# Kernel tuning notes

Measured on AMD Instinct MI355X. Metric: run time of the kernel, lower is better.

The kernel has to match this reference:

```python
import jax, jax.numpy as jnp
import numpy as np

V = 20000   # input_size (POI vocab)
U = 10000   # user_count
H = 128     # hidden_size
B = 64      # user_len (batch)
S = 200     # seq_len
LAM_T = 0.01
LAM_S = 100.0
DAY = 86400.0


def setup_inputs() -> dict:
    key = jax.random.key(0)
    ks = jax.random.split(key, 12)
    sc = 1.0 / np.sqrt(H)
    return {
        "poi_inputs": jax.random.randint(ks[0], (B, S), 0, V),
        "lengths": jnp.full((B,), S, dtype=jnp.int32),  # full sequences -> pack/pad is identity
        "timestamp_inputs": jnp.sort(jax.random.uniform(ks[1], (B, S), minval=0.0, maxval=DAY), axis=1),
        "location_inputs": jax.random.normal(ks[2], (B, S, 2)) * 0.1,
        "active_user": jax.random.randint(ks[3], (B,), 0, U),
        "emb_W": jax.random.normal(ks[4], (V, H)),      # nn.Embedding default N(0,1)
        "user_W": jax.random.normal(ks[5], (U, H)),
        "W_ih": jax.random.uniform(ks[6], (H, H), minval=-sc, maxval=sc),
        "W_hh": jax.random.uniform(ks[7], (H, H), minval=-sc, maxval=sc),
        "b_ih": jax.random.uniform(ks[8], (H,), minval=-sc, maxval=sc),
        "b_hh": jax.random.uniform(ks[9], (H,), minval=-sc, maxval=sc),
        "fc_W": jax.random.uniform(ks[10], (V, 2 * H), minval=-sc, maxval=sc),  # torch Linear [out,in]
        "fc_b": jax.random.uniform(ks[11], (V,), minval=-sc, maxval=sc),
    }


def _safe_norm(d):
    # norm over last axis with zero (not nan) gradient at d == 0
    d2 = jnp.sum(d * d, axis=-1)
    pos = d2 > 0
    return jnp.where(pos, jnp.sqrt(jnp.where(pos, d2, 1.0)), 0.0)


def reference(poi_inputs, lengths, timestamp_inputs, location_inputs, active_user,
              emb_W, user_W, W_ih, W_hh, b_ih, b_hh, fc_W, fc_b):
    t, s = timestamp_inputs, location_inputs
    x_emb = emb_W[poi_inputs]                       # [B,S,H]

    # vanilla tanh RNN (torch nn.RNN, batch_first) via scan over time
    def step(h, xt):
        h = jnp.tanh(xt @ W_ih.T + b_ih + h @ W_hh.T + b_hh)
        return h, h
    h0 = jnp.zeros((x_emb.shape[0], W_hh.shape[0]), x_emb.dtype)
    _, out = jax.lax.scan(step, h0, jnp.swapaxes(x_emb, 0, 1))
    out = jnp.swapaxes(out, 0, 1)                   # [B,S,H]

    # vectorized spatio-temporal decay attention (original O(S^2) python loop)
    dt = jnp.maximum(t[:, :, None] - t[:, None, :], 0.0)          # [B,S,S] clamp_min(0)
    ds = _safe_norm(s[:, :, None, :] - s[:, None, :, :])          # [B,S,S]
    a_j = ((jnp.cos(dt * (2.0 * jnp.pi / DAY)) + 1.0) * 0.5) * jnp.exp(-dt * LAM_T)
    b_j = jnp.exp(-ds * LAM_S)
    causal = jnp.tril(jnp.ones((t.shape[1], t.shape[1]), bool))   # j <= i
    w = jnp.where(causal, a_j * b_j + 1e-10, 0.0)                 # [B,S,S]
    sum_w = jnp.maximum(jnp.sum(w, axis=-1), 1e-10)               # [B,S]
    out_w = jnp.einsum('bij,bjh->bih', w, out) / sum_w[..., None] # [B,S,H]

    p_u = jnp.broadcast_to(user_W[active_user][:, None, :], out_w.shape)
    out_pu = jnp.concatenate([out_w, p_u], axis=-1)               # [B,S,2H]
    y = jax.nn.softmax(out_pu @ fc_W.T + fc_b, axis=-1)           # [B,S,V]
    return y, out_pu
```

## Files before the change

kernel.cpp:

```cpp
#include <hip/hip_runtime.h>
#include <hip/hip_bf16.h>
#include <stdint.h>

#define B_   64
#define S_   200
#define H_   128
#define V_   20000
#define M_   12800
#define NPAD 20224
#define NBN  158
#define NBM  100
#define NWG2 15800

#define WS_A      0u
#define WS_FCW    3276800u
#define WS_U      8454144u
#define WS_RSUM   13631488u
#define WS_WTIH   13682688u

#define XP_OFF    0
#define HOUT_OFF  2000000
#define PART_OFF  4000000
#define OUTPU_OFF 256000000ll

typedef __attribute__((ext_vector_type(8))) __bf16 bf16x8;
typedef __attribute__((ext_vector_type(4))) float  f32x4;

__device__ __forceinline__ void gll16(const void* g, void* l) {
  __builtin_amdgcn_global_load_lds(
      (const __attribute__((address_space(1))) void*)g,
      (__attribute__((address_space(3))) void*)l, 16, 0, 0);
}

__global__ __launch_bounds__(256)
void prep_w1(const float* __restrict__ fcw, __hip_bfloat16* __restrict__ w1) {
  int t = threadIdx.x;
  int row = blockIdx.x * 2 + (t >> 7);
  int col = t & 127;
  float v = (row < V_) ? fcw[(long)row * 256 + col] : 0.f;
  w1[(long)row * 128 + col] = __float2bfloat16(v);
}

__global__ __launch_bounds__(128)
void prep_wt(const float* __restrict__ w_ih, float* __restrict__ wt) {
  int bid = blockIdx.x, t = threadIdx.x;
  wt[bid * 128 + t] = w_ih[t * 128 + bid];
}

__global__ __launch_bounds__(256)
void user_k(const int* __restrict__ auser, const float* __restrict__ userW,
            const float* __restrict__ fcW, const float* __restrict__ fcb,
            float* __restrict__ U) {
  __shared__ float uw[8][128];
  int t = threadIdx.x;
  int c = blockIdx.x * 256 + t;
  int b0 = blockIdx.y * 8;
  for (int i = t; i < 8 * 128; i += 256) {
    int bb = i >> 7, kk = i & 127;
    uw[bb][kk] = userW[(long)auser[b0 + bb] * 128 + kk];
  }
  __syncthreads();
  float acc[8];
#pragma unroll
  for (int bb = 0; bb < 8; ++bb) acc[bb] = 0.f;
  if (c < V_) {
    const float* w2 = fcW + (long)c * 256 + 128;
    for (int kq = 0; kq < 32; ++kq) {
      float4 wv = *(const float4*)(w2 + 4 * kq);
#pragma unroll
      for (int bb = 0; bb < 8; ++bb) {
        float4 uv = *(const float4*)&uw[bb][4 * kq];
        acc[bb] = fmaf(wv.x, uv.x, acc[bb]);
        acc[bb] = fmaf(wv.y, uv.y, acc[bb]);
        acc[bb] = fmaf(wv.z, uv.z, acc[bb]);
        acc[bb] = fmaf(wv.w, uv.w, acc[bb]);
      }
    }
    float base = fcb[c];
#pragma unroll
    for (int bb = 0; bb < 8; ++bb)
      U[(long)(b0 + bb) * NPAD + c] = base + acc[bb];
  } else {
#pragma unroll
    for (int bb = 0; bb < 8; ++bb)
      U[(long)(b0 + bb) * NPAD + c] = -1e30f;
  }
}

__global__ __launch_bounds__(128)
void xproj_k(const int* __restrict__ poi, const float* __restrict__ emb,
             const float* __restrict__ wt_ih, const float* __restrict__ b_ih,
             const float* __restrict__ b_hh, float* __restrict__ xp) {
  __shared__ float xs[16][128];
  int j = threadIdx.x;
  int m0 = blockIdx.x * 16;
#pragma unroll
  for (int i = 0; i < 16; ++i)
    xs[i][j] = emb[(long)poi[m0 + i] * 128 + j];
  __syncthreads();
  float bias = b_ih[j] + b_hh[j];
  float acc[16];
#pragma unroll
  for (int i = 0; i < 16; ++i) acc[i] = bias;
  for (int kq = 0; kq < 32; ++kq) {
    float w0 = wt_ih[(4 * kq + 0) * 128 + j];
    float w1 = wt_ih[(4 * kq + 1) * 128 + j];
    float w2 = wt_ih[(4 * kq + 2) * 128 + j];
    float w3 = wt_ih[(4 * kq + 3) * 128 + j];
#pragma unroll
    for (int i = 0; i < 16; ++i) {
      float4 xv = *(const float4*)&xs[i][4 * kq];
      acc[i] = fmaf(xv.x, w0, acc[i]);
      acc[i] = fmaf(xv.y, w1, acc[i]);
      acc[i] = fmaf(xv.z, w2, acc[i]);
      acc[i] = fmaf(xv.w, w3, acc[i]);
    }
  }
#pragma unroll
  for (int i = 0; i < 16; ++i)
    xp[(long)(m0 + i) * 128 + j] = acc[i];
}

__global__ __launch_bounds__(128)
void rnn_k(const float* __restrict__ xp, const float* __restrict__ w_hh,
           float* __restrict__ hout) {
  int b = blockIdx.x, j = threadIdx.x;
  float w[128];
#pragma unroll
  for (int k = 0; k < 128; ++k) w[k] = w_hh[j * 128 + k];
  __shared__ float hs[2][128];
  hs[0][j] = 0.f;
  __syncthreads();
  int cur = 0;
  for (int t = 0; t < S_; ++t) {
    float x0 = xp[((long)b * S_ + t) * 128 + j];
    const float4* hp4 = (const float4*)hs[cur];
    float a0 = 0.f, a1 = 0.f, a2 = 0.f, a3 = 0.f;
#pragma unroll
    for (int k = 0; k < 8; ++k) {
      float4 v0 = hp4[k], v1 = hp4[k + 8], v2 = hp4[k + 16], v3 = hp4[k + 24];
      a0 = fmaf(v0.x, w[4 * k + 0], a0); a0 = fmaf(v0.y, w[4 * k + 1], a0);
      a0 = fmaf(v0.z, w[4 * k + 2], a0); a0 = fmaf(v0.w, w[4 * k + 3], a0);
      a1 = fmaf(v1.x, w[32 + 4 * k + 0], a1); a1 = fmaf(v1.y, w[32 + 4 * k + 1], a1);
      a1 = fmaf(v1.z, w[32 + 4 * k + 2], a1); a1 = fmaf(v1.w, w[32 + 4 * k + 3], a1);
      a2 = fmaf(v2.x, w[64 + 4 * k + 0], a2); a2 = fmaf(v2.y, w[64 + 4 * k + 1], a2);
      a2 = fmaf(v2.z, w[64 + 4 * k + 2], a2); a2 = fmaf(v2.w, w[64 + 4 * k + 3], a2);
      a3 = fmaf(v3.x, w[96 + 4 * k + 0], a3); a3 = fmaf(v3.y, w[96 + 4 * k + 1], a3);
      a3 = fmaf(v3.z, w[96 + 4 * k + 2], a3); a3 = fmaf(v3.w, w[96 + 4 * k + 3], a3);
    }
    float hn = tanhf(x0 + ((a0 + a1) + (a2 + a3)));
    hs[cur ^ 1][j] = hn;
    hout[((long)b * S_ + t) * 128 + j] = hn;
    cur ^= 1;
    __syncthreads();
  }
}

__global__ __launch_bounds__(128)
void attn_k(const float* __restrict__ ts, const float* __restrict__ loc,
            const float* __restrict__ hout, const int* __restrict__ auser,
            const float* __restrict__ userW, float* __restrict__ outpu,
            __hip_bfloat16* __restrict__ Abf) {
  int i = blockIdx.x, b = blockIdx.y, h = threadIdx.x;
  __shared__ float wl[128];
  const float OMEGA = 7.27220521664304e-05f;
  float ti = ts[b * S_ + i];
  float lx = loc[(b * S_ + i) * 2 + 0];
  float ly = loc[(b * S_ + i) * 2 + 1];
  float acc = 0.f, sw = 0.f;
  for (int jc = 0; jc <= i; jc += 128) {
    int j = jc + h;
    float wj = 0.f;
    if (j <= i) {
      float dt = fmaxf(ti - ts[b * S_ + j], 0.f);
      float a = (cosf(dt * OMEGA) + 1.f) * 0.5f * expf(-dt * 0.01f);
      float dx = lx - loc[(b * S_ + j) * 2 + 0];
      float dy = ly - loc[(b * S_ + j) * 2 + 1];
      float dn = sqrtf(dx * dx + dy * dy);
      wj = a * expf(-dn * 100.f) + 1e-10f;
    }
    __syncthreads();
    wl[h] = wj;
    __syncthreads();
    int lim = min(128, i - jc + 1);
    const float* hb = hout + ((long)b * S_ + jc) * 128 + h;
    int jj = 0;
    for (; jj + 4 <= lim; jj += 4) {
      float4 wv4 = *(const float4*)&wl[jj];
      float h0 = hb[(long)(jj + 0) * 128];
      float h1 = hb[(long)(jj + 1) * 128];
      float h2 = hb[(long)(jj + 2) * 128];
      float h3 = hb[(long)(jj + 3) * 128];
      acc = fmaf(wv4.x, h0, acc); sw += wv4.x;
      acc = fmaf(wv4.y, h1, acc); sw += wv4.y;
      acc = fmaf(wv4.z, h2, acc); sw += wv4.z;
      acc = fmaf(wv4.w, h3, acc); sw += wv4.w;
    }
    for (; jj < lim; ++jj) {
      float wv = wl[jj];
      acc = fmaf(wv, hb[(long)jj * 128], acc);
      sw += wv;
    }
  }
  float ow = acc / fmaxf(sw, 1e-10f);
  long m = (long)b * S_ + i;
  float pu = userW[(long)auser[b] * 128 + h];
  outpu[m * 256 + h]       = ow;
  outpu[m * 256 + 128 + h] = pu;
  Abf[m * 128 + h]         = __float2bfloat16(ow);
}

template <int PASS>
__global__ __launch_bounds__(512, 4)
void gemm_fc(const __hip_bfloat16* __restrict__ A,
             const __hip_bfloat16* __restrict__ Bw,
             const float* __restrict__ Ut,
             const float* __restrict__ rowsum,
             float* __restrict__ part,
             float* __restrict__ y) {
  __shared__ __align__(16) char smem[65536];
  __shared__ float rsum4[4][128];
  char* AsB = smem;
  char* BsB = smem + 32768;
  float* lbuf = (float*)smem;

  const int tid  = threadIdx.x;
  const int lane = tid & 63;
  const int wid  = tid >> 6;
  const int wr = wid >> 2, wc = wid & 3;
  const int g = lane >> 4, lr = lane & 15;

  const int orig = blockIdx.x;
  const int nid = (orig & 7) * (NWG2 / 8) + (orig >> 3);
  const int bm = nid / NBN, bn = nid % NBN;
  const long brow = (long)bm * 128, bcol = (long)bn * 128;

  const char* Ab = (const char*)A + brow * 256;
  const char* Bb = (const char*)Bw + bcol * 256;

#pragma unroll
  for (int i = 0; i < 4; ++i) {
    int ci = i * 512 + tid;
    int row = ci >> 4;
    int w = (ci & 15) ^ (row & 7);
    long src = (long)row * 256 + (long)w * 16;
    gll16(Ab + src, AsB + (long)ci * 16);
    gll16(Bb + src, BsB + (long)ci * 16);
  }
  __syncthreads();

  f32x4 acc[4][2];
#pragma unroll
  for (int mi = 0; mi < 4; ++mi)
#pragma unroll
    for (int ni = 0; ni < 2; ++ni) acc[mi][ni] = (f32x4)(0.f);

#pragma unroll
  for (int kk = 0; kk < 4; ++kk) {
    bf16x8 af[4], bfr[2];
#pragma unroll
    for (int mi = 0; mi < 4; ++mi) {
      int row = wr * 64 + mi * 16 + lr;
      int w = ((kk << 2) | g) ^ (row & 7);
      af[mi] = *(const bf16x8*)(AsB + row * 256 + w * 16);
    }
#pragma unroll
    for (int ni = 0; ni < 2; ++ni) {
      int row = wc * 32 + ni * 16 + lr;
      int w = ((kk << 2) | g) ^ (row & 7);
      bfr[ni] = *(const bf16x8*)(BsB + row * 256 + w * 16);
    }
#pragma unroll
    for (int mi = 0; mi < 4; ++mi)
#pragma unroll
      for (int ni = 0; ni < 2; ++ni)
        acc[mi][ni] = __builtin_amdgcn_mfma_f32_16x16x32_bf16(af[mi], bfr[ni], acc[mi][ni], 0, 0, 0);
  }

  if (PASS == 0) {
#pragma unroll
    for (int mi = 0; mi < 4; ++mi) {
#pragma unroll
      for (int r = 0; r < 4; ++r) {
        long row = brow + wr * 64 + mi * 16 + g * 4 + r;
        const float* urow = Ut + (long)(row / S_) * NPAD + bcol;
        float s = 0.f;
#pragma unroll
        for (int ni = 0; ni < 2; ++ni) {
          float u = urow[wc * 32 + ni * 16 + lr];
          s += __expf(acc[mi][ni][r] + u);
        }
#pragma unroll
        for (int off = 1; off < 16; off <<= 1) s += __shfl_xor(s, off);
        if (lr == 0) rsum4[wc][wr * 64 + mi * 16 + g * 4 + r] = s;
      }
    }
    __syncthreads();
    if (tid < 128)
      part[(long)bn * M_ + brow + tid] =
          rsum4[0][tid] + rsum4[1][tid] + rsum4[2][tid] + rsum4[3][tid];
  } else {
    if (bcol >= V_) return;
    const bool full = (bcol + 128 <= V_);
    __syncthreads();
#pragma unroll
    for (int mi = 0; mi < 4; ++mi) {
#pragma unroll
      for (int r = 0; r < 4; ++r) {
        int lrow = wr * 64 + mi * 16 + g * 4 + r;
        long row = brow + lrow;
        const float* urow = Ut + (long)(row / S_) * NPAD + bcol;
        float inv = 1.0f / rowsum[row];
        int key = ((lrow >> 2) & 3) << 2;
#pragma unroll
        for (int ni = 0; ni < 2; ++ni) {
          int lcol = wc * 32 + ni * 16 + lr;
          lbuf[lrow * 128 + (lcol ^ key)] = __expf(acc[mi][ni][r] + urow[lcol]) * inv;
        }
      }
    }
    __syncthreads();
    if (full) {
#pragma unroll
      for (int it = 0; it < 8; ++it) {
        int idx = it * 512 + tid;
        int lrow = idx >> 5, c4 = idx & 31;
        int key = ((lrow >> 2) & 3) << 2;
        f32x4 v = *(const f32x4*)(lbuf + lrow * 128 + ((c4 * 4) ^ key));
        __builtin_nontemporal_store(v,
            (f32x4*)(y + (brow + lrow) * (long)V_ + bcol + c4 * 4));
      }
    } else {
#pragma unroll
      for (int it = 0; it < 8; ++it) {
        int idx = it * 512 + tid;
        int lrow = idx >> 5, c4 = idx & 31;
        int key = ((lrow >> 2) & 3) << 2;
        const float* src = lbuf + lrow * 128 + ((c4 * 4) ^ key);
        long row = brow + lrow;
#pragma unroll
        for (int e = 0; e < 4; ++e) {
          int col = (int)bcol + c4 * 4 + e;
          if (col < V_) y[row * (long)V_ + col] = src[e];
        }
      }
    }
  }
}

__global__ void reduce_rows(const float* __restrict__ part, float* __restrict__ rowsum) {
  int m = blockIdx.x * 256 + threadIdx.x;
  if (m < M_) {
    float s = 0.f;
    for (int bn = 0; bn < NBN; ++bn) s += part[(long)bn * M_ + m];
    rowsum[m] = fmaxf(s, 1e-30f);
  }
}

extern "C" void kernel_launch(void* const* d_in, const int* in_sizes, int n_in,
                              void* d_out, int out_size, void* d_ws, size_t ws_size,
                              hipStream_t stream) {
  const int*   poi   = (const int*)d_in[0];
  const float* ts    = (const float*)d_in[2];
  const float* loc   = (const float*)d_in[3];
  const int*   auser = (const int*)d_in[4];
  const float* embW  = (const float*)d_in[5];
  const float* userW = (const float*)d_in[6];
  const float* w_ih  = (const float*)d_in[7];
  const float* w_hh  = (const float*)d_in[8];
  const float* b_ih  = (const float*)d_in[9];
  const float* b_hh  = (const float*)d_in[10];
  const float* fcW   = (const float*)d_in[11];
  const float* fcb   = (const float*)d_in[12];

  float* out = (float*)d_out;
  char*  ws  = (char*)d_ws;
  __hip_bfloat16* Abf    = (__hip_bfloat16*)(ws + WS_A);
  __hip_bfloat16* w1b    = (__hip_bfloat16*)(ws + WS_FCW);
  float*          Ut     = (float*)(ws + WS_U);
  float*          rowsum = (float*)(ws + WS_RSUM);
  float*          wt_ih  = (float*)(ws + WS_WTIH);

  float* xp    = out + XP_OFF;
  float* hout  = out + HOUT_OFF;
  float* part  = out + PART_OFF;
  float* outpu = out + OUTPU_OFF;

  prep_w1<<<dim3(NPAD / 2), dim3(256), 0, stream>>>(fcW, w1b);
  prep_wt<<<dim3(128), dim3(128), 0, stream>>>(w_ih, wt_ih);
  user_k<<<dim3(NPAD / 256, 8), dim3(256), 0, stream>>>(auser, userW, fcW, fcb, Ut);
  xproj_k<<<dim3(M_ / 16), dim3(128), 0, stream>>>(poi, embW, wt_ih, b_ih, b_hh, xp);
  rnn_k<<<dim3(B_), dim3(128), 0, stream>>>(xp, w_hh, hout);
  attn_k<<<dim3(S_, B_), dim3(128), 0, stream>>>(ts, loc, hout, auser, userW, outpu, Abf);
  gemm_fc<0><<<dim3(NWG2), dim3(512), 0, stream>>>(Abf, w1b, Ut, nullptr, part, nullptr);
  reduce_rows<<<dim3(50), dim3(256), 0, stream>>>(part, rowsum);
  gemm_fc<1><<<dim3(NWG2), dim3(512), 0, stream>>>(Abf, w1b, Ut, rowsum, nullptr, out);
}
```

Before: 762.6 us.

## Tile attention over 8 query rows with shared-memory hidden tile; remap GEMM block order

```diff
diff --git a/kernel.cpp b/kernel.cpp
--- a/kernel.cpp
+++ b/kernel.cpp
@@ -11,6 +11,7 @@
 #define NBN  158
 #define NBM  100
 #define NWG2 15800
+#define TI   8
 
 #define WS_A      0u
 #define WS_FCW    3276800u
@@ -161,53 +162,69 @@
             const float* __restrict__ hout, const int* __restrict__ auser,
             const float* __restrict__ userW, float* __restrict__ outpu,
             __hip_bfloat16* __restrict__ Abf) {
-  int i = blockIdx.x, b = blockIdx.y, h = threadIdx.x;
-  __shared__ float wl[128];
+  int it = blockIdx.x, b = blockIdx.y, h = threadIdx.x;
+  int i0 = it * TI;
+  __shared__ float htile[128 * 128];
+  __shared__ float wls[TI][128];
   const float OMEGA = 7.27220521664304e-05f;
-  float ti = ts[b * S_ + i];
-  float lx = loc[(b * S_ + i) * 2 + 0];
-  float ly = loc[(b * S_ + i) * 2 + 1];
-  float acc = 0.f, sw = 0.f;
-  for (int jc = 0; jc <= i; jc += 128) {
+  float ti[TI], lx[TI], ly[TI], acc[TI], sw[TI];
+#pragma unroll
+  for (int ii = 0; ii < TI; ++ii) {
+    ti[ii] = ts[b * S_ + i0 + ii];
+    lx[ii] = loc[(b * S_ + i0 + ii) * 2 + 0];
+    ly[ii] = loc[(b * S_ + i0 + ii) * 2 + 1];
+    acc[ii] = 0.f; sw[ii] = 0.f;
+  }
+  for (int jc = 0; jc < i0 + TI; jc += 128) {
+    int nrows = min(128, i0 + TI - jc);
+    __syncthreads();
+    {
+      const float4* src = (const float4*)(hout + ((long)b * S_ + jc) * 128);
+      float4* dst = (float4*)htile;
+      int n4 = nrows * 32;
+      for (int idx = h; idx < n4; idx += 128) dst[idx] = src[idx];
+    }
     int j = jc + h;
-    float wj = 0.f;
-    if (j <= i) {
-      float dt = fmaxf(ti - ts[b * S_ + j], 0.f);
-      float a = (cosf(dt * OMEGA) + 1.f) * 0.5f * expf(-dt * 0.01f);
-      float dx = lx - loc[(b * S_ + j) * 2 + 0];
-      float dy = ly - loc[(b * S_ + j) * 2 + 1];
-      float dn = sqrtf(dx * dx + dy * dy);
-      wj = a * expf(-dn * 100.f) + 1e-10f;
-    }
-    __syncthreads();
-    wl[h] = wj;
-    __syncthreads();
-    int lim = min(128, i - jc + 1);
-    const float* hb = hout + ((long)b * S_ + jc) * 128 + h;
-    int jj = 0;
-    for (; jj + 4 <= lim; jj += 4) {
-      float4 wv4 = *(const float4*)&wl[jj];
-      float h0 = hb[(long)(jj + 0) * 128];
-      float h1 = hb[(long)(jj + 1) * 128];
-      float h2 = hb[(long)(jj + 2) * 128];
-      float h3 = hb[(long)(jj + 3) * 128];
-      acc = fmaf(wv4.x, h0, acc); sw += wv4.x;
-      acc = fmaf(wv4.y, h1, acc); sw += wv4.y;
-      acc = fmaf(wv4.z, h2, acc); sw += wv4.z;
-      acc = fmaf(wv4.w, h3, acc); sw += wv4.w;
-    }
-    for (; jj < lim; ++jj) {
-      float wv = wl[jj];
-      acc = fmaf(wv, hb[(long)jj * 128], acc);
-      sw += wv;
-    }
-  }
-  float ow = acc / fmaxf(sw, 1e-10f);
-  long m = (long)b * S_ + i;
+    float tj = ts[b * S_ + j < B_ * S_ ? b * S_ + j : 0];
+    float jx = 0.f, jy = 0.f;
+    if (j < S_) {
+      tj = ts[b * S_ + j];
+      jx = loc[(b * S_ + j) * 2 + 0];
+      jy = loc[(b * S_ + j) * 2 + 1];
+    }
+#pragma unroll
+    for (int ii = 0; ii < TI; ++ii) {
+      float wj = 0.f;
+      if (j <= i0 + ii) {
+        float dt = fmaxf(ti[ii] - tj, 0.f);
+        float a = (cosf(dt * OMEGA) + 1.f) * 0.5f * expf(-dt * 0.01f);
+        float dx = lx[ii] - jx;
+        float dy = ly[ii] - jy;
+        float dn = sqrtf(dx * dx + dy * dy);
+        wj = a * expf(-dn * 100.f) + 1e-10f;
+      }
+      wls[ii][h] = wj;
+    }
+    __syncthreads();
+#pragma unroll
+    for (int ii = 0; ii < TI; ++ii) {
+      int lim = min(nrows, i0 + ii - jc + 1);
+      for (int r = 0; r < lim; ++r) {
+        float wv = wls[ii][r];
+        acc[ii] = fmaf(wv, htile[r * 128 + h], acc[ii]);
+        sw[ii] += wv;
+      }
+    }
+  }
   float pu = userW[(long)auser[b] * 128 + h];
-  outpu[m * 256 + h]       = ow;
-  outpu[m * 256 + 128 + h] = pu;
-  Abf[m * 128 + h]         = __float2bfloat16(ow);
+#pragma unroll
+  for (int ii = 0; ii < TI; ++ii) {
+    long m = (long)b * S_ + i0 + ii;
+    float ow = acc[ii] / fmaxf(sw[ii], 1e-10f);
+    outpu[m * 256 + h]       = ow;
+    outpu[m * 256 + 128 + h] = pu;
+    Abf[m * 128 + h]         = __float2bfloat16(ow);
+  }
 }
 
 template <int PASS>
@@ -232,7 +249,7 @@
 
   const int orig = blockIdx.x;
   const int nid = (orig & 7) * (NWG2 / 8) + (orig >> 3);
-  const int bm = nid / NBN, bn = nid % NBN;
+  const int bn = nid / NBM, bm = nid % NBM;
   const long brow = (long)bm * 128, bcol = (long)bn * 128;
 
   const char* Ab = (const char*)A + brow * 256;
@@ -391,7 +408,7 @@
   user_k<<<dim3(NPAD / 256, 8), dim3(256), 0, stream>>>(auser, userW, fcW, fcb, Ut);
   xproj_k<<<dim3(M_ / 16), dim3(128), 0, stream>>>(poi, embW, wt_ih, b_ih, b_hh, xp);
   rnn_k<<<dim3(B_), dim3(128), 0, stream>>>(xp, w_hh, hout);
-  attn_k<<<dim3(S_, B_), dim3(128), 0, stream>>>(ts, loc, hout, auser, userW, outpu, Abf);
+  attn_k<<<dim3(S_ / TI, B_), dim3(128), 0, stream>>>(ts, loc, hout, auser, userW, outpu, Abf);
   gemm_fc<0><<<dim3(NWG2), dim3(512), 0, stream>>>(Abf, w1b, Ut, nullptr, part, nullptr);
   reduce_rows<<<dim3(50), dim3(256), 0, stream>>>(part, rowsum);
   gemm_fc<1><<<dim3(NWG2), dim3(512), 0, stream>>>(Abf, w1b, Ut, rowsum, nullptr, out);
```

Result: slower. 797.5 us (+4.6%).

## Fuse RNN, weight bf16 conversion and user projection into one heterogeneous launch

Applied to the files above, without the earlier changes.

```diff
diff --git a/kernel.cpp b/kernel.cpp
--- a/kernel.cpp
+++ b/kernel.cpp
@@ -32,59 +32,10 @@
       (__attribute__((address_space(3))) void*)l, 16, 0, 0);
 }
 
-__global__ __launch_bounds__(256)
-void prep_w1(const float* __restrict__ fcw, __hip_bfloat16* __restrict__ w1) {
-  int t = threadIdx.x;
-  int row = blockIdx.x * 2 + (t >> 7);
-  int col = t & 127;
-  float v = (row < V_) ? fcw[(long)row * 256 + col] : 0.f;
-  w1[(long)row * 128 + col] = __float2bfloat16(v);
-}
-
 __global__ __launch_bounds__(128)
 void prep_wt(const float* __restrict__ w_ih, float* __restrict__ wt) {
   int bid = blockIdx.x, t = threadIdx.x;
   wt[bid * 128 + t] = w_ih[t * 128 + bid];
-}
-
-__global__ __launch_bounds__(256)
-void user_k(const int* __restrict__ auser, const float* __restrict__ userW,
-            const float* __restrict__ fcW, const float* __restrict__ fcb,
-            float* __restrict__ U) {
-  __shared__ float uw[8][128];
-  int t = threadIdx.x;
-  int c = blockIdx.x * 256 + t;
-  int b0 = blockIdx.y * 8;
-  for (int i = t; i < 8 * 128; i += 256) {
-    int bb = i >> 7, kk = i & 127;
-    uw[bb][kk] = userW[(long)auser[b0 + bb] * 128 + kk];
-  }
-  __syncthreads();
-  float acc[8];
-#pragma unroll
-  for (int bb = 0; bb < 8; ++bb) acc[bb] = 0.f;
-  if (c < V_) {
-    const float* w2 = fcW + (long)c * 256 + 128;
-    for (int kq = 0; kq < 32; ++kq) {
-      float4 wv = *(const float4*)(w2 + 4 * kq);
-#pragma unroll
-      for (int bb = 0; bb < 8; ++bb) {
-        float4 uv = *(const float4*)&uw[bb][4 * kq];
-        acc[bb] = fmaf(wv.x, uv.x, acc[bb]);
-        acc[bb] = fmaf(wv.y, uv.y, acc[bb]);
-        acc[bb] = fmaf(wv.z, uv.z, acc[bb]);
-        acc[bb] = fmaf(wv.w, uv.w, acc[bb]);
-      }
-    }
-    float base = fcb[c];
-#pragma unroll
-    for (int bb = 0; bb < 8; ++bb)
-      U[(long)(b0 + bb) * NPAD + c] = base + acc[bb];
-  } else {
-#pragma unroll
-    for (int bb = 0; bb < 8; ++bb)
-      U[(long)(b0 + bb) * NPAD + c] = -1e30f;
-  }
 }
 
 __global__ __launch_bounds__(128)
@@ -121,38 +72,105 @@
     xp[(long)(m0 + i) * 128 + j] = acc[i];
 }
 
-__global__ __launch_bounds__(128)
-void rnn_k(const float* __restrict__ xp, const float* __restrict__ w_hh,
-           float* __restrict__ hout) {
-  int b = blockIdx.x, j = threadIdx.x;
-  float w[128];
-#pragma unroll
-  for (int k = 0; k < 128; ++k) w[k] = w_hh[j * 128 + k];
-  __shared__ float hs[2][128];
-  hs[0][j] = 0.f;
-  __syncthreads();
-  int cur = 0;
-  for (int t = 0; t < S_; ++t) {
-    float x0 = xp[((long)b * S_ + t) * 128 + j];
-    const float4* hp4 = (const float4*)hs[cur];
-    float a0 = 0.f, a1 = 0.f, a2 = 0.f, a3 = 0.f;
-#pragma unroll
-    for (int k = 0; k < 8; ++k) {
-      float4 v0 = hp4[k], v1 = hp4[k + 8], v2 = hp4[k + 16], v3 = hp4[k + 24];
-      a0 = fmaf(v0.x, w[4 * k + 0], a0); a0 = fmaf(v0.y, w[4 * k + 1], a0);
-      a0 = fmaf(v0.z, w[4 * k + 2], a0); a0 = fmaf(v0.w, w[4 * k + 3], a0);
-      a1 = fmaf(v1.x, w[32 + 4 * k + 0], a1); a1 = fmaf(v1.y, w[32 + 4 * k + 1], a1);
-      a1 = fmaf(v1.z, w[32 + 4 * k + 2], a1); a1 = fmaf(v1.w, w[32 + 4 * k + 3], a1);
-      a2 = fmaf(v2.x, w[64 + 4 * k + 0], a2); a2 = fmaf(v2.y, w[64 + 4 * k + 1], a2);
-      a2 = fmaf(v2.z, w[64 + 4 * k + 2], a2); a2 = fmaf(v2.w, w[64 + 4 * k + 3], a2);
-      a3 = fmaf(v3.x, w[96 + 4 * k + 0], a3); a3 = fmaf(v3.y, w[96 + 4 * k + 1], a3);
-      a3 = fmaf(v3.z, w[96 + 4 * k + 2], a3); a3 = fmaf(v3.w, w[96 + 4 * k + 3], a3);
-    }
-    float hn = tanhf(x0 + ((a0 + a1) + (a2 + a3)));
-    hs[cur ^ 1][j] = hn;
-    hout[((long)b * S_ + t) * 128 + j] = hn;
-    cur ^= 1;
-    __syncthreads();
+__global__ __launch_bounds__(256)
+void fused_pre(const float* __restrict__ xp, const float* __restrict__ w_hh,
+               float* __restrict__ hout,
+               const float* __restrict__ fcW, __hip_bfloat16* __restrict__ w1,
+               const int* __restrict__ auser, const float* __restrict__ userW,
+               const float* __restrict__ fcb, float* __restrict__ U) {
+  __shared__ float smem_u[8][128];
+  int blk = blockIdx.x;
+  int t = threadIdx.x;
+
+  if (blk < 64) {
+    int b = blk, j = t & 127;
+    float* hs = (float*)smem_u;
+    float w[128];
+#pragma unroll
+    for (int k = 0; k < 128; ++k) w[k] = w_hh[j * 128 + k];
+    hs[j] = 0.f;
+    __syncthreads();
+    int cur = 0;
+    for (int tt = 0; tt < S_; ++tt) {
+      float x0 = xp[((long)b * S_ + tt) * 128 + j];
+      const float4* hp4 = (const float4*)(hs + cur * 128);
+      float a0 = 0.f, a1 = 0.f, a2 = 0.f, a3 = 0.f;
+#pragma unroll
+      for (int k = 0; k < 8; ++k) {
+        float4 v0 = hp4[k], v1 = hp4[k + 8], v2 = hp4[k + 16], v3 = hp4[k + 24];
+        a0 = fmaf(v0.x, w[4 * k + 0], a0); a0 = fmaf(v0.y, w[4 * k + 1], a0);
+        a0 = fmaf(v0.z, w[4 * k + 2], a0); a0 = fmaf(v0.w, w[4 * k + 3], a0);
+        a1 = fmaf(v1.x, w[32 + 4 * k + 0], a1); a1 = fmaf(v1.y, w[32 + 4 * k + 1], a1);
+        a1 = fmaf(v1.z, w[32 + 4 * k + 2], a1); a1 = fmaf(v1.w, w[32 + 4 * k + 3], a1);
+        a2 = fmaf(v2.x, w[64 + 4 * k + 0], a2); a2 = fmaf(v2.y, w[64 + 4 * k + 1], a2);
+        a2 = fmaf(v2.z, w[64 + 4 * k + 2], a2); a2 = fmaf(v2.w, w[64 + 4 * k + 3], a2);
+        a3 = fmaf(v3.x, w[96 + 4 * k + 0], a3); a3 = fmaf(v3.y, w[96 + 4 * k + 1], a3);
+        a3 = fmaf(v3.z, w[96 + 4 * k + 2], a3); a3 = fmaf(v3.w, w[96 + 4 * k + 3], a3);
+      }
+      float hn = tanhf(x0 + ((a0 + a1) + (a2 + a3)));
+      hs[(cur ^ 1) * 128 + j] = hn;
+      hout[((long)b * S_ + tt) * 128 + j] = hn;
+      cur ^= 1;
+      __syncthreads();
+    }
+  } else if (blk < 222) {
+    int row = (blk - 64) * 128 + (t >> 1);
+    int c0 = (t & 1) * 64;
+    const float* src = fcW + (long)row * 256 + c0;
+    __hip_bfloat16* dst = w1 + (long)row * 128 + c0;
+    bool valid = row < V_;
+#pragma unroll
+    for (int q = 0; q < 8; ++q) {
+      float4 v0, v1;
+      if (valid) { v0 = *(const float4*)(src + q * 8); v1 = *(const float4*)(src + q * 8 + 4); }
+      else { v0 = make_float4(0.f, 0.f, 0.f, 0.f); v1 = v0; }
+      ushort4 p0, p1;
+      p0.x = __bfloat16_as_ushort(__float2bfloat16(v0.x));
+      p0.y = __bfloat16_as_ushort(__float2bfloat16(v0.y));
+      p0.z = __bfloat16_as_ushort(__float2bfloat16(v0.z));
+      p0.w = __bfloat16_as_ushort(__float2bfloat16(v0.w));
+      p1.x = __bfloat16_as_ushort(__float2bfloat16(v1.x));
+      p1.y = __bfloat16_as_ushort(__float2bfloat16(v1.y));
+      p1.z = __bfloat16_as_ushort(__float2bfloat16(v1.z));
+      p1.w = __bfloat16_as_ushort(__float2bfloat16(v1.w));
+      *(ushort4*)(dst + q * 8)     = p0;
+      *(ushort4*)(dst + q * 8 + 4) = p1;
+    }
+  } else {
+    int idx = blk - 222;
+    int cb = idx % 79, bgrp = idx / 79;
+    int c = cb * 256 + t;
+    int b0 = bgrp * 8;
+    for (int i = t; i < 8 * 128; i += 256) {
+      int bb = i >> 7, kk = i & 127;
+      smem_u[bb][kk] = userW[(long)auser[b0 + bb] * 128 + kk];
+    }
+    __syncthreads();
+    float acc[8];
+#pragma unroll
+    for (int bb = 0; bb < 8; ++bb) acc[bb] = 0.f;
+    if (c < V_) {
+      const float* w2 = fcW + (long)c * 256 + 128;
+      for (int kq = 0; kq < 32; ++kq) {
+        float4 wv = *(const float4*)(w2 + 4 * kq);
+#pragma unroll
+        for (int bb = 0; bb < 8; ++bb) {
+          float4 uv = *(const float4*)&smem_u[bb][4 * kq];
+          acc[bb] = fmaf(wv.x, uv.x, acc[bb]);
+          acc[bb] = fmaf(wv.y, uv.y, acc[bb]);
+          acc[bb] = fmaf(wv.z, uv.z, acc[bb]);
+          acc[bb] = fmaf(wv.w, uv.w, acc[bb]);
+        }
+      }
+      float base = fcb[c];
+#pragma unroll
+      for (int bb = 0; bb < 8; ++bb)
+        U[(long)(b0 + bb) * NPAD + c] = base + acc[bb];
+    } else {
+#pragma unroll
+      for (int bb = 0; bb < 8; ++bb)
+        U[(long)(b0 + bb) * NPAD + c] = -1e30f;
+    }
   }
 }
 
@@ -232,7 +250,7 @@
 
   const int orig = blockIdx.x;
   const int nid = (orig & 7) * (NWG2 / 8) + (orig >> 3);
-  const int bm = nid / NBN, bn = nid % NBN;
+  const int bn = nid / NBM, bm = nid % NBM;
   const long brow = (long)bm * 128, bcol = (long)bn * 128;
 
   const char* Ab = (const char*)A + brow * 256;
@@ -386,11 +404,10 @@
   float* part  = out + PART_OFF;
   float* outpu = out + OUTPU_OFF;
 
-  prep_w1<<<dim3(NPAD / 2), dim3(256), 0, stream>>>(fcW, w1b);
   prep_wt<<<dim3(128), dim3(128), 0, stream>>>(w_ih, wt_ih);
-  user_k<<<dim3(NPAD / 256, 8), dim3(256), 0, stream>>>(auser, userW, fcW, fcb, Ut);
   xproj_k<<<dim3(M_ / 16), dim3(128), 0, stream>>>(poi, embW, wt_ih, b_ih, b_hh, xp);
-  rnn_k<<<dim3(B_), dim3(128), 0, stream>>>(xp, w_hh, hout);
+  fused_pre<<<dim3(64 + 158 + 632), dim3(256), 0, stream>>>(
+      xp, w_hh, hout, fcW, w1b, auser, userW, fcb, Ut);
   attn_k<<<dim3(S_, B_), dim3(128), 0, stream>>>(ts, loc, hout, auser, userW, outpu, Abf);
   gemm_fc<0><<<dim3(NWG2), dim3(512), 0, stream>>>(Abf, w1b, Ut, nullptr, part, nullptr);
   reduce_rows<<<dim3(50), dim3(256), 0, stream>>>(part, rowsum);
```

Measured after the change: 734.7 us. -3.7%, faster.
